# Kernel optimization log

Hardware: AMD Instinct MI355X
Metric: run time of the kernel (lower is better)

Reference implementation:

```python
import jax, jax.numpy as jnp
import numpy as np

B, T, U = 8, 256, 64
ENC_DIM, DEC_DIM, JOINT_DIM, VOCAB = 512, 512, 640, 1024


def setup_inputs() -> dict:
    key = jax.random.key(0)
    k1, k2, k3, k4, k5 = jax.random.split(key, 5)
    s_enc = 1.0 / np.sqrt(ENC_DIM)
    s_dec = 1.0 / np.sqrt(DEC_DIM)
    s_joint = 1.0 / np.sqrt(JOINT_DIM)
    return {
        "enc_out": jax.random.normal(k1, (B, T, ENC_DIM), dtype=jnp.float32),
        "pred_out": jax.random.normal(k2, (B, U, DEC_DIM), dtype=jnp.float32),
        # nn.Linear weights stored as [out, in], applied as x @ W.T
        "W_enc": jax.random.uniform(k3, (JOINT_DIM, ENC_DIM), jnp.float32, -s_enc, s_enc),
        "W_pred": jax.random.uniform(k4, (JOINT_DIM, DEC_DIM), jnp.float32, -s_dec, s_dec),
        "W_out": jax.random.uniform(k5, (VOCAB, JOINT_DIM), jnp.float32, -s_joint, s_joint),
    }


def reference(enc_out, pred_out, W_enc, W_pred, W_out):
    # project: [B,T,J] and [B,U,J]
    enc_p = jnp.einsum("bte,je->btj", enc_out, W_enc)
    pred_p = jnp.einsum("bud,jd->buj", pred_out, W_pred)
    # broadcast add -> [B,T,U,J], SiLU, then output GEMM -> [B,T,U,V]
    joint = enc_p[:, :, None, :] + pred_p[:, None, :, :]
    joint = joint * jax.nn.sigmoid(joint)  # SiLU
    out = jnp.einsum("btuj,vj->btuv", joint, W_out)
    return out
```

## Files before the change

### kernel.cpp

```cpp
#include <hip/hip_runtime.h>

typedef unsigned short u16;
typedef __attribute__((ext_vector_type(8))) short short8;
typedef __attribute__((ext_vector_type(8))) unsigned short ushort8v;
typedef __attribute__((ext_vector_type(4))) float f32x4;

#define B_ 8
#define T_ 256
#define U_ 64
#define E_ 512
#define J_ 640
#define V_ 1024
#define NT 20

__device__ __forceinline__ u16 f2bf(float f) {
  unsigned int u = __float_as_uint(f);
  u += 0x7fffu + ((u >> 16) & 1u);
  return (u16)(u >> 16);
}

__device__ __forceinline__ void gload16(const void* g, void* l) {
  __builtin_amdgcn_global_load_lds((const __attribute__((address_space(1))) void*)g,
                                   (__attribute__((address_space(3))) void*)l,
                                   16, 0, 0);
}

__global__ __launch_bounds__(256) void cast5_k(const float4* __restrict__ s0,
                                               const float4* __restrict__ s1,
                                               const float4* __restrict__ s2,
                                               const float4* __restrict__ s3,
                                               const float4* __restrict__ s4,
                                               ushort4* __restrict__ dst) {
  int i = blockIdx.x * 256 + threadIdx.x;
  const int st = gridDim.x * 256;
  for (; i < 655360; i += st) {
    const float4* s; int off;
    if (i < 262144)      { s = s0; off = 0; }
    else if (i < 327680) { s = s1; off = 262144; }
    else if (i < 409600) { s = s2; off = 327680; }
    else if (i < 491520) { s = s3; off = 409600; }
    else                 { s = s4; off = 491520; }
    float4 v = s[i - off];
    ushort4 o;
    o.x = f2bf(v.x); o.y = f2bf(v.y); o.z = f2bf(v.z); o.w = f2bf(v.w);
    dst[i] = o;
  }
}

__global__ __launch_bounds__(256) void proj_k(const u16* __restrict__ X,
                                              const u16* __restrict__ W,
                                              float* __restrict__ C) {
  __shared__ __align__(16) u16 As[128 * 32];
  __shared__ __align__(16) u16 Bs[128 * 32];
  const int tid = threadIdx.x;
  const int w = tid >> 6, lane = tid & 63;
  const int wr = w >> 1, wc = w & 1;
  const int m0 = blockIdx.x * 128, n0 = blockIdx.y * 128;
  const int lr = lane & 15, lk = lane >> 4;
  const int r4 = tid >> 2, kq = tid & 3;

  f32x4 acc[4][4] = {};

  for (int ks = 0; ks < E_ / 32; ++ks) {
    const int k0 = ks * 32;
    gload16(X + (size_t)(m0 + r4) * E_ + k0 + kq * 8, (char*)As + w * 1024);
    gload16(X + (size_t)(m0 + 64 + r4) * E_ + k0 + kq * 8, (char*)As + 4096 + w * 1024);
    gload16(W + (size_t)(n0 + r4) * E_ + k0 + kq * 8, (char*)Bs + w * 1024);
    gload16(W + (size_t)(n0 + 64 + r4) * E_ + k0 + kq * 8, (char*)Bs + 4096 + w * 1024);
    __syncthreads();
    short8 a[4], bb[4];
#pragma unroll
    for (int m = 0; m < 4; ++m)
      a[m] = *(const short8*)&As[(wr * 64 + m * 16 + lr) * 32 + lk * 8];
#pragma unroll
    for (int n = 0; n < 4; ++n)
      bb[n] = *(const short8*)&Bs[(wc * 64 + n * 16 + lr) * 32 + lk * 8];
#pragma unroll
    for (int m = 0; m < 4; ++m)
#pragma unroll
      for (int n = 0; n < 4; ++n)
        acc[m][n] = __builtin_amdgcn_mfma_f32_16x16x32_bf16(a[m], bb[n], acc[m][n], 0, 0, 0);
    __syncthreads();
  }

#pragma unroll
  for (int m = 0; m < 4; ++m) {
    const int row = m0 + wr * 64 + m * 16 + lk * 4;
#pragma unroll
    for (int n = 0; n < 4; ++n) {
      const int col = n0 + wc * 64 + n * 16 + lr;
#pragma unroll
      for (int i = 0; i < 4; ++i)
        C[(size_t)(row + i) * J_ + col] = acc[m][n][i];
    }
  }
}

__global__ __launch_bounds__(256) void pack_k(const u16* __restrict__ Wo,
                                              u16* __restrict__ pk) {
  const int u = blockIdx.x * 256 + threadIdx.x;
  const int l = u & 63;
  int r = u >> 6;
  const int nq = r & 3;  r >>= 2;
  const int ks = r % 20;
  const int vt = r / 20;
  const int v = vt * 64 + nq * 16 + (l & 15);
  const int k = ks * 32 + (l >> 4) * 8;
  *(short8*)(pk + (size_t)u * 8) = *(const short8*)(Wo + (size_t)v * J_ + k);
}

__global__ __launch_bounds__(512, 2) void fused2_k(const float* __restrict__ ep,
                                                   const float* __restrict__ pp,
                                                   const u16* __restrict__ pk,
                                                   float* __restrict__ out) {
  __shared__ __align__(16) u16 Alds[64 * 640];
  const int tid = threadIdx.x;
  const int w = tid >> 6, lane = tid & 63;
  const int lr = lane & 15, lk = lane >> 4;
  const int bt = blockIdx.x;
  const int b = bt >> 8;
  const size_t m0 = (size_t)bt * 64;

  const float* eprow = ep + (size_t)bt * J_;
  const float* pbase = pp + (size_t)b * 64 * J_;
#pragma unroll
  for (int it = 0; it < 10; ++it) {
    const int unit = tid + it * 512;
    const int row = unit / 80;
    const int c = unit - row * 80;
    union { float4 v[2]; float f[8]; } Ee, Pp;
    Ee.v[0] = *(const float4*)(eprow + c * 8);
    Ee.v[1] = *(const float4*)(eprow + c * 8 + 4);
    Pp.v[0] = *(const float4*)(pbase + (size_t)row * J_ + c * 8);
    Pp.v[1] = *(const float4*)(pbase + (size_t)row * J_ + c * 8 + 4);
    union { ushort8v v; u16 s[8]; } R;
#pragma unroll
    for (int j = 0; j < 8; ++j) {
      float x = Ee.f[j] + Pp.f[j];
      R.s[j] = f2bf(x * __builtin_amdgcn_rcpf(1.0f + __expf(-x)));
    }
    *(ushort8v*)&Alds[row * 640 + ((c ^ (row & 7)) << 3)] = R.v;
  }
  __syncthreads();

  const int rx = lr & 7;
  int arow[4];
#pragma unroll
  for (int mq = 0; mq < 4; ++mq) arow[mq] = (mq * 16 + lr) * 640;

#define AR(aF, ks)                                                             \
  do {                                                                         \
    _Pragma("unroll")                                                          \
    for (int mq = 0; mq < 4; ++mq)                                             \
      aF[mq] = *(const short8*)&Alds[arow[mq] + ((((ks) * 4 + lk) ^ rx) << 3)];\
  } while (0)

#define BL(bF, ks)                                                             \
  do {                                                                         \
    _Pragma("unroll")                                                          \
    for (int nq = 0; nq < 4; ++nq)                                             \
      bF[nq] = *(const short8*)(bp + (ks) * 2048 + nq * 512);                  \
  } while (0)

#define MM(aF, bF)                                                             \
  do {                                                                         \
    __builtin_amdgcn_s_setprio(1);                                             \
    _Pragma("unroll")                                                          \
    for (int mq = 0; mq < 4; ++mq)                                             \
      _Pragma("unroll")                                                        \
      for (int nq = 0; nq < 4; ++nq)                                           \
        acc[mq][nq] = __builtin_amdgcn_mfma_f32_16x16x32_bf16(aF[mq], bF[nq],  \
                                                              acc[mq][nq], 0, 0, 0); \
    __builtin_amdgcn_s_setprio(0);                                             \
  } while (0)

#pragma unroll 1
  for (int c2 = 0; c2 < 2; ++c2) {
    const int vt = w * 2 + c2;
    const int col0 = vt * 64;
    const u16* bp = pk + (size_t)vt * 40960 + lane * 8;

    f32x4 acc[4][4] = {};
    short8 B0[4], B1[4], B2[4], B3[4], aE[4], aO[4];
    BL(B0, 0); BL(B1, 1);
    AR(aE, 0);
#pragma unroll 1
    for (int ks = 0; ks < NT; ks += 4) {
      BL(B2, ks + 2); AR(aO, ks + 1); MM(aE, B0);
      BL(B3, ks + 3); AR(aE, ks + 2); MM(aO, B1);
      if (ks + 4 < NT) BL(B0, ks + 4);
      AR(aO, ks + 3); MM(aE, B2);
      if (ks + 4 < NT) { BL(B1, ks + 5); AR(aE, ks + 4); }
      MM(aO, B3);
    }

#pragma unroll
    for (int mq = 0; mq < 4; ++mq) {
      const size_t row = m0 + mq * 16 + lk * 4;
#pragma unroll
      for (int nq = 0; nq < 4; ++nq) {
        const int col = col0 + nq * 16 + lr;
#pragma unroll
        for (int i = 0; i < 4; ++i)
          out[(row + i) * V_ + col] = acc[mq][nq][i];
      }
    }
  }
#undef AR
#undef BL
#undef MM
}

extern "C" void kernel_launch(void* const* d_in, const int* in_sizes, int n_in,
                              void* d_out, int out_size, void* d_ws, size_t ws_size,
                              hipStream_t stream) {
  const float* enc = (const float*)d_in[0];
  const float* pred = (const float*)d_in[1];
  const float* We = (const float*)d_in[2];
  const float* Wp = (const float*)d_in[3];
  const float* Wo = (const float*)d_in[4];
  float* out = (float*)d_out;

  char* ws = (char*)d_ws;
  u16* enc_bf = (u16*)ws;
  u16* pred_bf = (u16*)(ws + 2097152);
  u16* We_bf = (u16*)(ws + 2621440);
  u16* Wp_bf = (u16*)(ws + 3276800);
  u16* Wo_bf = (u16*)(ws + 3932160);
  float* ep = (float*)(ws + 5242880);
  float* pp = (float*)(ws + 10485760);
  u16* Wo_pk = (u16*)(ws + 11796480);

  cast5_k<<<2048, 256, 0, stream>>>((const float4*)enc, (const float4*)pred,
                                    (const float4*)We, (const float4*)Wp,
                                    (const float4*)Wo, (ushort4*)ws);

  proj_k<<<dim3(16, 5), 256, 0, stream>>>(enc_bf, We_bf, ep);
  proj_k<<<dim3(4, 5), 256, 0, stream>>>(pred_bf, Wp_bf, pp);
  pack_k<<<320, 256, 0, stream>>>(Wo_bf, Wo_pk);

  fused2_k<<<2048, 512, 0, stream>>>(ep, pp, Wo_pk, out);
}
```

Measured before the change: 238.2 us.

## Merge projection launches, fuse Wo cast into pack, unroll main loop, drop setprio

The two projection GEMM launches become a single grid that picks the encoder or predictor operands by block index. The W_out bf16 cast now happens inside the packing kernel, which removes an intermediate buffer and a pass over it. In the main fused kernel the K loop is fully unrolled and the s_setprio hints around the MFMA groups are removed. The goal is fewer launches and less small-kernel overhead, plus better scheduling in the dominant kernel, at the cost of more register pressure and code size from the unroll.

```diff
diff --git a/kernel.cpp b/kernel.cpp
--- a/kernel.cpp
+++ b/kernel.cpp
@@ -25,21 +25,19 @@
                                    16, 0, 0);
 }
 
-__global__ __launch_bounds__(256) void cast5_k(const float4* __restrict__ s0,
+__global__ __launch_bounds__(256) void cast4_k(const float4* __restrict__ s0,
                                                const float4* __restrict__ s1,
                                                const float4* __restrict__ s2,
                                                const float4* __restrict__ s3,
-                                               const float4* __restrict__ s4,
                                                ushort4* __restrict__ dst) {
   int i = blockIdx.x * 256 + threadIdx.x;
   const int st = gridDim.x * 256;
-  for (; i < 655360; i += st) {
+  for (; i < 491520; i += st) {
     const float4* s; int off;
     if (i < 262144)      { s = s0; off = 0; }
     else if (i < 327680) { s = s1; off = 262144; }
     else if (i < 409600) { s = s2; off = 327680; }
-    else if (i < 491520) { s = s3; off = 409600; }
-    else                 { s = s4; off = 491520; }
+    else                 { s = s3; off = 409600; }
     float4 v = s[i - off];
     ushort4 o;
     o.x = f2bf(v.x); o.y = f2bf(v.y); o.z = f2bf(v.z); o.w = f2bf(v.w);
@@ -47,15 +45,40 @@
   }
 }
 
-__global__ __launch_bounds__(256) void proj_k(const u16* __restrict__ X,
-                                              const u16* __restrict__ W,
-                                              float* __restrict__ C) {
+__global__ __launch_bounds__(256) void packf_k(const float* __restrict__ Wo,
+                                               u16* __restrict__ pk) {
+  const int u = blockIdx.x * 256 + threadIdx.x;
+  const int l = u & 63;
+  int r = u >> 6;
+  const int nq = r & 3;  r >>= 2;
+  const int ks = r % 20;
+  const int vt = r / 20;
+  const int v = vt * 64 + nq * 16 + (l & 15);
+  const int k = ks * 32 + (l >> 4) * 8;
+  const float* src = Wo + (size_t)v * J_ + k;
+  union { ushort8v vv; u16 s[8]; } R;
+#pragma unroll
+  for (int j = 0; j < 8; ++j) R.s[j] = f2bf(src[j]);
+  *(ushort8v*)(pk + (size_t)u * 8) = R.vv;
+}
+
+__global__ __launch_bounds__(256) void proj2_k(const u16* __restrict__ Xe,
+                                               const u16* __restrict__ Xp,
+                                               const u16* __restrict__ We,
+                                               const u16* __restrict__ Wp,
+                                               float* __restrict__ Ce,
+                                               float* __restrict__ Cp) {
   __shared__ __align__(16) u16 As[128 * 32];
   __shared__ __align__(16) u16 Bs[128 * 32];
   const int tid = threadIdx.x;
   const int w = tid >> 6, lane = tid & 63;
   const int wr = w >> 1, wc = w & 1;
-  const int m0 = blockIdx.x * 128, n0 = blockIdx.y * 128;
+  const bool isE = blockIdx.x < 16;
+  const u16* X = isE ? Xe : Xp;
+  const u16* W = isE ? We : Wp;
+  float* C = isE ? Ce : Cp;
+  const int m0 = (isE ? blockIdx.x : blockIdx.x - 16) * 128;
+  const int n0 = blockIdx.y * 128;
   const int lr = lane & 15, lk = lane >> 4;
   const int r4 = tid >> 2, kq = tid & 3;
 
@@ -94,19 +117,6 @@
         C[(size_t)(row + i) * J_ + col] = acc[m][n][i];
     }
   }
-}
-
-__global__ __launch_bounds__(256) void pack_k(const u16* __restrict__ Wo,
-                                              u16* __restrict__ pk) {
-  const int u = blockIdx.x * 256 + threadIdx.x;
-  const int l = u & 63;
-  int r = u >> 6;
-  const int nq = r & 3;  r >>= 2;
-  const int ks = r % 20;
-  const int vt = r / 20;
-  const int v = vt * 64 + nq * 16 + (l & 15);
-  const int k = ks * 32 + (l >> 4) * 8;
-  *(short8*)(pk + (size_t)u * 8) = *(const short8*)(Wo + (size_t)v * J_ + k);
 }
 
 __global__ __launch_bounds__(512, 2) void fused2_k(const float* __restrict__ ep,
@@ -164,14 +174,12 @@
 
 #define MM(aF, bF)                                                             \
   do {                                                                         \
-    __builtin_amdgcn_s_setprio(1);                                             \
     _Pragma("unroll")                                                          \
     for (int mq = 0; mq < 4; ++mq)                                             \
       _Pragma("unroll")                                                        \
       for (int nq = 0; nq < 4; ++nq)                                           \
         acc[mq][nq] = __builtin_amdgcn_mfma_f32_16x16x32_bf16(aF[mq], bF[nq],  \
                                                               acc[mq][nq], 0, 0, 0); \
-    __builtin_amdgcn_s_setprio(0);                                             \
   } while (0)
 
 #pragma unroll 1
@@ -184,7 +192,7 @@
     short8 B0[4], B1[4], B2[4], B3[4], aE[4], aO[4];
     BL(B0, 0); BL(B1, 1);
     AR(aE, 0);
-#pragma unroll 1
+#pragma unroll
     for (int ks = 0; ks < NT; ks += 4) {
       BL(B2, ks + 2); AR(aO, ks + 1); MM(aE, B0);
       BL(B3, ks + 3); AR(aE, ks + 2); MM(aO, B1);
@@ -226,18 +234,16 @@
   u16* pred_bf = (u16*)(ws + 2097152);
   u16* We_bf = (u16*)(ws + 2621440);
   u16* Wp_bf = (u16*)(ws + 3276800);
-  u16* Wo_bf = (u16*)(ws + 3932160);
   float* ep = (float*)(ws + 5242880);
   float* pp = (float*)(ws + 10485760);
   u16* Wo_pk = (u16*)(ws + 11796480);
 
-  cast5_k<<<2048, 256, 0, stream>>>((const float4*)enc, (const float4*)pred,
+  cast4_k<<<1920, 256, 0, stream>>>((const float4*)enc, (const float4*)pred,
                                     (const float4*)We, (const float4*)Wp,
-                                    (const float4*)Wo, (ushort4*)ws);
-
-  proj_k<<<dim3(16, 5), 256, 0, stream>>>(enc_bf, We_bf, ep);
-  proj_k<<<dim3(4, 5), 256, 0, stream>>>(pred_bf, Wp_bf, pp);
-  pack_k<<<320, 256, 0, stream>>>(Wo_bf, Wo_pk);
+                                    (ushort4*)ws);
+  packf_k<<<320, 256, 0, stream>>>(Wo, Wo_pk);
+
+  proj2_k<<<dim3(20, 5), 256, 0, stream>>>(enc_bf, pred_bf, We_bf, Wp_bf, ep, pp);
 
   fused2_k<<<2048, 512, 0, stream>>>(ep, pp, Wo_pk, out);
 }
```

Measured after the change: 676.5 us. 2.84x slower.
